# Optimization experiments

Measured on AMD Instinct MI355X. Metric: run time of the kernel, lower is better.

Reference implementation:

```python
import jax, jax.numpy as jnp
import numpy as np
import math

N, LQ, C, HD, L, P = 2, 17821, 256, 8, 4, 4
D = C // HD
SHAPES = [(100, 134), (50, 67), (25, 34), (13, 17)]


def setup_inputs() -> dict:
    key = jax.random.key(0)
    ks = jax.random.split(key, 8)
    shapes = np.array(SHAPES, np.int32)
    areas = shapes[:, 0] * shapes[:, 1]
    starts = np.concatenate([[0], np.cumsum(areas)[:-1]]).astype(np.int32)
    Lin = int(areas.sum())
    sc = 1.0 / math.sqrt(C)
    # sampling_offsets bias: radial grid init as in _reset_parameters
    thetas = np.arange(HD, dtype=np.float32) * (2.0 * math.pi / HD)
    grid = np.stack([np.cos(thetas), np.sin(thetas)], -1)
    grid = grid / np.abs(grid).max(-1, keepdims=True)
    grid = np.tile(grid[:, None, None, :], (1, L, P, 1)) * np.arange(1, P + 1, dtype=np.float32)[None, None, :, None]
    boff = jnp.asarray(grid.reshape(-1), jnp.float32)
    return dict(
        query=jax.random.normal(ks[0], (N, LQ, C), jnp.float32),
        reference_points=jax.random.uniform(ks[1], (N, LQ, L, 2), jnp.float32),
        input_flatten=jax.random.normal(ks[2], (N, Lin, C), jnp.float32),
        input_spatial_shapes=jnp.asarray(shapes),
        input_level_start_index=jnp.asarray(starts),
        Wv=jax.random.normal(ks[3], (C, C), jnp.float32) * sc,
        bv=jnp.zeros((C,), jnp.float32),
        Woff=jax.random.normal(ks[4], (C, HD * L * P * 2), jnp.float32) * 0.01,
        boff=boff,
        Watt=jax.random.normal(ks[5], (C, HD * L * P), jnp.float32) * 0.02,
        batt=jnp.zeros((HD * L * P,), jnp.float32),
        Wout=jax.random.normal(ks[6], (C, C), jnp.float32) * sc,
        bout=jnp.zeros((C,), jnp.float32),
    )


def _ms_deform_attn_core(value, shapes, starts, loc, attw):
    # value: (N, Len_in, HD, D); loc: (N, Lq, HD, L, P, 2) in [0,1]; attw: (N, Lq, HD, L, P)
    n, lq = loc.shape[0], loc.shape[1]
    out = jnp.zeros((n, lq, HD, D), value.dtype)
    for l in range(L):
        H, W = int(shapes[l, 0]), int(shapes[l, 1])
        s = int(starts[l])
        v = value[:, s:s + H * W]                                    # (N, HW, HD, D)
        # (N,Lq,HD,P,2) -> (N,Lq,P,HD,2) -> (N,Lq*P,HD) per coord
        locl = loc[:, :, :, l].transpose(0, 1, 3, 2, 4).reshape(n, lq * P, HD, 2)
        # grid_sample align_corners=False mapping
        x = locl[..., 0] * W - 0.5
        y = locl[..., 1] * H - 0.5
        x0f, y0f = jnp.floor(x), jnp.floor(y)
        fx, fy = x - x0f, y - y0f
        x0, y0 = x0f.astype(jnp.int32), y0f.astype(jnp.int32)

        def corner(xi, yi, w):
            valid = (xi >= 0) & (xi < W) & (yi >= 0) & (yi < H)      # zero padding
            idx = jnp.clip(yi, 0, H - 1) * W + jnp.clip(xi, 0, W - 1)
            g = jnp.take_along_axis(v, idx[..., None], axis=1)        # (N, Lq*P, HD, D)
            return g * (w * valid)[..., None]

        samp = (corner(x0, y0, (1 - fx) * (1 - fy))
                + corner(x0 + 1, y0, fx * (1 - fy))
                + corner(x0, y0 + 1, (1 - fx) * fy)
                + corner(x0 + 1, y0 + 1, fx * fy))                    # (N, Lq*P, HD, D)
        aw = attw[:, :, :, l].transpose(0, 1, 3, 2).reshape(n, lq * P, HD)
        out = out + (samp * aw[..., None]).reshape(n, lq, P, HD, D).sum(axis=2)
    return out.reshape(n, lq, HD * D)


def reference(query, reference_points, input_flatten, input_spatial_shapes,
              input_level_start_index, Wv, bv, Woff, boff, Watt, batt, Wout, bout):
    shapes = np.asarray(input_spatial_shapes)
    starts = np.asarray(input_level_start_index)
    n, lq, _ = query.shape
    value = (input_flatten @ Wv + bv).reshape(n, -1, HD, D)
    offsets = (query @ Woff + boff).reshape(n, lq, HD, L, P, 2)
    # reference_points has last dim 2 -> normalize offsets by (W, H) per level
    norm = jnp.asarray(shapes[:, ::-1], jnp.float32)                  # (L, 2) = (W, H)
    loc = reference_points[:, :, None, :, None, :] + offsets / norm[None, None, None, :, None, :]
    attw = (query @ Watt + batt).reshape(n, lq, HD, L * P)
    attw = jax.nn.softmax(attw, axis=-1).reshape(n, lq, HD, L, P)
    out = _ms_deform_attn_core(value, shapes, starts, loc, attw)
    return out @ Wout + bout
```

## Files before the change

kernel.cpp:

```cpp
#include <hip/hip_runtime.h>
#include <hip/hip_bf16.h>
#include <math.h>

#define NB    2
#define LQ    17821
#define LIN   17821
#define CCH   256
#define HDN   8
#define DCH   32
#define LVL   4
#define NPT   4
#define KDIM  256
#define QCH   16
#define NCHUNK ((LQ + QCH - 1) / QCH)

__constant__ const int   cH[LVL]  = {100, 50, 25, 13};
__constant__ const int   cW[LVL]  = {134, 67, 34, 17};
__constant__ const int   cS[LVL]  = {0, 13400, 16750, 17600};
__constant__ const float cHf[LVL] = {100.f, 50.f, 25.f, 13.f};
__constant__ const float cWf[LVL] = {134.f, 67.f, 34.f, 17.f};
__constant__ const float cRH[LVL] = {1.f/100.f, 1.f/50.f, 1.f/25.f, 1.f/13.f};
__constant__ const float cRW[LVL] = {1.f/134.f, 1.f/67.f, 1.f/34.f, 1.f/17.f};

typedef __attribute__((ext_vector_type(8))) _Float16 f16x8;
typedef __attribute__((ext_vector_type(4))) _Float16 f16x4;
typedef __attribute__((ext_vector_type(2))) _Float16 f16x2;
typedef __attribute__((ext_vector_type(4))) float    f32x4;

__device__ __forceinline__ void glds16(const void* g, void* l) {
    __builtin_amdgcn_global_load_lds(
        (const __attribute__((address_space(1))) void*)g,
        (__attribute__((address_space(3))) void*)l, 16, 0, 0);
}

__device__ __forceinline__ int packw(float w) {
    const unsigned short b = __builtin_bit_cast(unsigned short, (_Float16)w);
    return (int)((unsigned)b * 0x10001u);
}

__global__ void prep_all(const float* __restrict__ Wv,
                         const float* __restrict__ Woff,
                         const float* __restrict__ Watt,
                         const float* __restrict__ Wout,
                         const float* __restrict__ boff,
                         const float* __restrict__ batt,
                         _Float16* __restrict__ wvT,
                         _Float16* __restrict__ wqT,
                         _Float16* __restrict__ wuT,
                         float* __restrict__ b384)
{
    const int i = blockIdx.x * 256 + threadIdx.x;
    if (i < 65536) {
        const int n = i >> 8, k = i & 255;
        wvT[i] = (_Float16)Wv[(size_t)k * 256 + n];
    } else if (i < 131072) {
        const int j = i - 65536, n = j >> 8, k = j & 255;
        wqT[j] = (_Float16)Woff[(size_t)k * 256 + n];
    } else if (i < 163840) {
        const int j = i - 131072, n = j >> 8, k = j & 255;
        wqT[65536 + j] = (_Float16)Watt[(size_t)k * 128 + n];
    } else if (i < 229376) {
        const int j = i - 163840, n = j >> 8, k = j & 255;
        wuT[j] = (_Float16)Wout[(size_t)k * 256 + n];
    } else {
        const int j = i - 229376;
        if (j < 256)      b384[j] = boff[j];
        else if (j < 384) b384[j] = batt[j - 256];
    }
}

template<typename AT, typename OutT, bool PERM>
__device__ __forceinline__ void gemm_body(
    _Float16* AsBase, _Float16* BsBase,
    const AT* __restrict__ A,
    const _Float16* __restrict__ BT,
    const float* __restrict__ bias, OutT* __restrict__ C,
    int M, int Ntot, int bx, int by)
{
    const int t    = threadIdx.x;
    const int wav  = t >> 6;
    const int lane = t & 63;
    const int bm   = by * 128;
    const int bn   = bx * 128;

    const int wr = wav >> 1, wc = wav & 1;
    const int fcol = lane & 15;
    const int fk   = lane >> 4;

    int aoff[4], boff[4];
#pragma unroll
    for (int i = 0; i < 4; ++i) {
        const int ar = wr * 64 + i * 16 + fcol;
        aoff[i] = ar * 64 + ((fk ^ ((ar >> 1) & 3)) << 4);
        const int br = wc * 64 + i * 16 + fcol;
        boff[i] = br * 64 + ((fk ^ ((br >> 1) & 3)) << 4);
    }

    const int srow = lane >> 2;
    const int slot = lane & 3;

    f32x4 acc[4][4];
#pragma unroll
    for (int i = 0; i < 4; ++i)
#pragma unroll
        for (int j = 0; j < 4; ++j) acc[i][j] = (f32x4)(0.f);

    auto stage = [&](int s, int buf) {
        _Float16* As = AsBase + buf * 4096;
        _Float16* Bs = BsBase + buf * 4096;
#pragma unroll
        for (int i = 0; i < 2; ++i) {
            const int j   = wav + i * 4;
            const int row = j * 16 + srow;
            const int swz = ((row >> 1) & 3) << 4;
            const int rga = min(bm + row, M - 1);
            if constexpr (sizeof(AT) == 2) {
                const int kb = (slot << 4) ^ swz;
                glds16((const char*)A + (size_t)rga * 512 + s * 64 + kb,
                       (char*)As + j * 1024);
            } else {
                const char* src = (const char*)A + (size_t)rga * 1024 + s * 128 + slot * 32;
                const float4 u0 = *reinterpret_cast<const float4*>(src);
                const float4 u1 = *reinterpret_cast<const float4*>(src + 16);
                f16x8 hv;
                hv[0] = (_Float16)u0.x; hv[1] = (_Float16)u0.y;
                hv[2] = (_Float16)u0.z; hv[3] = (_Float16)u0.w;
                hv[4] = (_Float16)u1.x; hv[5] = (_Float16)u1.y;
                hv[6] = (_Float16)u1.z; hv[7] = (_Float16)u1.w;
                *reinterpret_cast<f16x8*>((char*)As + j * 1024 + srow * 64
                                          + ((slot << 4) ^ swz)) = hv;
            }
            {
                const int kb = (slot << 4) ^ swz;
                const int rgb = bn + row;
                glds16((const char*)BT + (size_t)rgb * 512 + s * 64 + kb,
                       (char*)Bs + j * 1024);
            }
        }
    };

    stage(0, 0);
    asm volatile("s_waitcnt vmcnt(0) lgkmcnt(0)" ::: "memory");
    __builtin_amdgcn_s_barrier();

    int cur = 0;
#pragma unroll 1
    for (int s = 0; s < 8; ++s) {
        if (s + 1 < 8) {
            stage(s + 1, cur ^ 1);
            if constexpr (sizeof(AT) == 2)
                asm volatile("s_waitcnt vmcnt(4)" ::: "memory");
            else
                asm volatile("s_waitcnt vmcnt(6)" ::: "memory");
            __builtin_amdgcn_sched_barrier(0);
            __builtin_amdgcn_s_barrier();
        }
        const char* As = (const char*)(AsBase + cur * 4096);
        const char* Bs = (const char*)(BsBase + cur * 4096);
        f16x8 af[4], bfr[4];
#pragma unroll
        for (int i = 0; i < 4; ++i) {
            af[i]  = *reinterpret_cast<const f16x8*>(As + aoff[i]);
            bfr[i] = *reinterpret_cast<const f16x8*>(Bs + boff[i]);
        }
        asm volatile("s_waitcnt lgkmcnt(0)" ::: "memory");
        __builtin_amdgcn_sched_barrier(0);
#pragma unroll
        for (int mi = 0; mi < 4; ++mi)
#pragma unroll
            for (int ni = 0; ni < 4; ++ni)
                acc[mi][ni] = __builtin_amdgcn_mfma_f32_16x16x32_f16(
                    af[mi], bfr[ni], acc[mi][ni], 0, 0, 0);
        if (s + 1 < 8)
            __builtin_amdgcn_s_barrier();
        cur ^= 1;
    }

    const int r0 = bm + wr * 64 + (lane >> 4) * 4;
    const int c0 = bn + wc * 64 + fcol;
#pragma unroll
    for (int ni = 0; ni < 4; ++ni) {
        const int col = c0 + ni * 16;
        const float bv = bias[col];
#pragma unroll
        for (int mi = 0; mi < 4; ++mi) {
#pragma unroll
            for (int j = 0; j < 4; ++j) {
                const int r = r0 + mi * 16 + j;
                if (r < M) {
                    const float v = acc[mi][ni][j] + bv;
                    if (PERM) {
                        const int n   = (r >= LIN) ? 1 : 0;
                        const int pos = r - n * LIN;
                        const size_t dst = ((size_t)(n * HDN + (col >> 5)) * LIN + pos) * 32 + (col & 31);
                        C[dst] = (OutT)v;
                    } else {
                        C[(size_t)r * Ntot + col] = (OutT)v;
                    }
                }
            }
        }
    }
}

__global__ __launch_bounds__(256, 3) void gemm_fused2(
    const float* __restrict__ A0, const _Float16* __restrict__ BT0,
    const float* __restrict__ b0, _Float16* __restrict__ C0,
    const float* __restrict__ A1, const _Float16* __restrict__ BT1,
    const float* __restrict__ b1, _Float16* __restrict__ C1, int M)
{
    __shared__ _Float16 As[2][4096];
    __shared__ _Float16 Bs[2][4096];
    if (blockIdx.x < 2)
        gemm_body<float, _Float16, true >(&As[0][0], &Bs[0][0], A0, BT0, b0, C0,
                                          M, 256, blockIdx.x, blockIdx.y);
    else
        gemm_body<float, _Float16, false>(&As[0][0], &Bs[0][0], A1, BT1, b1, C1,
                                          M, 384, blockIdx.x - 2, blockIdx.y);
}

__global__ __launch_bounds__(256, 3) void gemm_out(
    const _Float16* __restrict__ A, const _Float16* __restrict__ BT,
    const float* __restrict__ bias, float* __restrict__ C, int M)
{
    __shared__ _Float16 As[2][4096];
    __shared__ _Float16 Bs[2][4096];
    gemm_body<_Float16, float, false>(&As[0][0], &Bs[0][0], A, BT, bias, C,
                                      M, 256, blockIdx.x, blockIdx.y);
}

__global__ __launch_bounds__(256) void msda_sample(
    const _Float16* __restrict__ value,
    const _Float16* __restrict__ qproj,
    const float* __restrict__ refp,
    _Float16* __restrict__ o16)
{
    __shared__ int2 sIW[QCH * 81 + 4];

    const int t   = threadIdx.x;
    const int bid = blockIdx.x;
    const int chunk = bid % NCHUNK;
    const int nh    = bid / NCHUNK;
    const int h     = nh & 7;
    const int n     = nh >> 3;

    {
        const int q1 = t >> 4;
        const int ip = t & 15;
        const int l  = ip >> 2;

        const int rq  = min(chunk * QCH + q1, LQ - 1);
        const int row = n * LQ + rq;
        const _Float16* qrow = qproj + (size_t)row * 384;

        const float logit = (float)qrow[256 + h * 16 + ip];
        float m = logit;
#pragma unroll
        for (int k = 8; k >= 1; k >>= 1) m = fmaxf(m, __shfl_xor(m, k));
        const float e = __expf(logit - m);
        float s = e;
#pragma unroll
        for (int k = 8; k >= 1; k >>= 1) s += __shfl_xor(s, k);
        const float aw = e / s;

        const float ox = (float)qrow[h * 32 + ip * 2 + 0];
        const float oy = (float)qrow[h * 32 + ip * 2 + 1];
        const float rx = refp[(size_t)row * 8 + l * 2 + 0];
        const float ry = refp[(size_t)row * 8 + l * 2 + 1];

        const int   Ww = cW[l], Hh = cH[l], st = cS[l];
        const float Wf = cWf[l], Hf = cHf[l];
        const float rW = cRW[l], rH = cRH[l];

        const float x = (rx + ox * rW) * Wf - 0.5f;
        const float y = (ry + oy * rH) * Hf - 0.5f;
        const float x0f = floorf(x);
        const float y0f = floorf(y);
        const float fx = x - x0f;
        const float fy = y - y0f;
        const int x0 = (int)x0f, y0 = (int)y0f;
        const int x1 = x0 + 1,   y1 = y0 + 1;

        const bool vx0 = (x0 >= 0) & (x0 < Ww);
        const bool vx1 = (x1 >= 0) & (x1 < Ww);
        const bool vy0 = (y0 >= 0) & (y0 < Hh);
        const bool vy1 = (y1 >= 0) & (y1 < Hh);

        const float gx0 = 1.f - fx, gx1 = fx;
        const float gy0 = 1.f - fy, gy1 = fy;

        const float w00 = (vx0 & vy0) ? gx0 * gy0 * aw : 0.f;
        const float w10 = (vx1 & vy0) ? gx1 * gy0 * aw : 0.f;
        const float w01 = (vx0 & vy1) ? gx0 * gy1 * aw : 0.f;
        const float w11 = (vx1 & vy1) ? gx1 * gy1 * aw : 0.f;

        const int xc0 = min(max(x0, 0), Ww - 1);
        const int xc1 = min(max(x1, 0), Ww - 1);
        const int yc0 = min(max(y0, 0), Hh - 1);
        const int yc1 = min(max(y1, 0), Hh - 1);

        const int base = (nh * LIN + st) * 64;
        const int b0   = q1 * 81 + ip * 5;
        sIW[b0 + 0] = make_int2(base + (yc0 * Ww + xc0) * 64, packw(w00));
        sIW[b0 + 1] = make_int2(base + (yc0 * Ww + xc1) * 64, packw(w10));
        sIW[b0 + 2] = make_int2(base + (yc1 * Ww + xc0) * 64, packw(w01));
        sIW[b0 + 3] = make_int2(base + (yc1 * Ww + xc1) * 64, packw(w11));
    }

    __syncthreads();

    const int q1  = t >> 4;
    const int lv  = (t >> 2) & 3;
    const int sub = t & 3;
    const char* vbase = (const char*)value + sub * 16;

    int2 iw[4][4];
#pragma unroll
    for (int i = 0; i < 4; ++i)
#pragma unroll
        for (int c = 0; c < 4; ++c)
            iw[i][c] = sIW[q1 * 81 + (lv * 4 + i) * 5 + c];

    f16x8 v[4][4];
#pragma unroll
    for (int i = 0; i < 4; ++i)
#pragma unroll
        for (int c = 0; c < 4; ++c)
            v[i][c] = *reinterpret_cast<const f16x8*>(vbase + iw[i][c].x);

    __builtin_amdgcn_sched_barrier(0);

    f16x2 acc2[4] = {};
#pragma unroll
    for (int i = 0; i < 4; ++i) {
#pragma unroll
        for (int c = 0; c < 4; ++c) {
            const f16x2 w2 = __builtin_bit_cast(f16x2, iw[i][c].y);
            const f16x2* v2 = reinterpret_cast<const f16x2*>(&v[i][c]);
#pragma unroll
            for (int j = 0; j < 4; ++j)
                acc2[j] = __builtin_elementwise_fma(v2[j], w2, acc2[j]);
        }
    }

    float acc[8];
#pragma unroll
    for (int j = 0; j < 4; ++j) {
        acc[2 * j]     = (float)acc2[j][0];
        acc[2 * j + 1] = (float)acc2[j][1];
    }

#pragma unroll
    for (int k = 4; k <= 8; k <<= 1)
#pragma unroll
        for (int j = 0; j < 8; ++j)
            acc[j] += __shfl_xor(acc[j], k);

    if ((t & 12) == 0) {
        const int rq  = min(chunk * QCH + q1, LQ - 1);
        const int row = n * LQ + rq;
        const size_t o = (size_t)row * 256 + h * 32 + sub * 8;
        f16x8 hv;
#pragma unroll
        for (int j = 0; j < 8; ++j) hv[j] = (_Float16)acc[j];
        *reinterpret_cast<f16x8*>(&o16[o]) = hv;
    }
}

extern "C" void kernel_launch(void* const* d_in, const int* in_sizes, int n_in,
                              void* d_out, int out_size, void* d_ws, size_t ws_size,
                              hipStream_t stream)
{
    const float* query  = (const float*)d_in[0];
    const float* refp   = (const float*)d_in[1];
    const float* inflat = (const float*)d_in[2];
    const float* Wv     = (const float*)d_in[5];
    const float* bv     = (const float*)d_in[6];
    const float* Woff   = (const float*)d_in[7];
    const float* boff   = (const float*)d_in[8];
    const float* Watt   = (const float*)d_in[9];
    const float* batt   = (const float*)d_in[10];
    const float* Wout   = (const float*)d_in[11];
    const float* bout   = (const float*)d_in[12];
    float* out = (float*)d_out;

    const int M = NB * LQ;
    const size_t MC = (size_t)M * 256;

    float* ws   = (float*)d_ws;
    float* b384 = ws;

    _Float16* fbase = (_Float16*)(b384 + 384);
    _Float16* qp16  = fbase;
    _Float16* v16   = qp16 + (size_t)M * 384;
    _Float16* o16   = v16 + MC;
    _Float16* wvT   = o16 + MC;
    _Float16* wqT   = wvT + 65536;
    _Float16* wuT   = wqT + 98304;

    const dim3 blk(256);
    const int mblk = (M + 127) / 128;

    prep_all<<<dim3(898), blk, 0, stream>>>(Wv, Woff, Watt, Wout, boff, batt,
                                            wvT, wqT, wuT, b384);

    gemm_fused2<<<dim3(5, mblk), blk, 0, stream>>>(
        inflat, wvT, bv, v16,
        query,  wqT, b384, qp16, M);

    msda_sample<<<dim3(NB * HDN * NCHUNK), blk, 0, stream>>>(v16, qp16, refp, o16);

    gemm_out<<<dim3(2, mblk), blk, 0, stream>>>(o16, wuT, bout, out, M);
}
```

Measured before the change: 158.9 us.

## Retile GEMMs to 64-row blocks spanning full output width per block

Replaces the 128x128 GEMM tiles with 64-row tiles covering 256 columns (or 192 for the query projection) per block, with each wavefront owning a column slice. A is then read once per row block instead of once per column tile, which cuts redundant fp32 input reads and the fp16 conversions that go with them. The fp32 A loads are software-pipelined into registers and written to shared memory after the MFMA step, and the barrier and waitcnt placement is reorganised to match. In exchange, each wave does fewer MFMAs per A fragment, blocks use more shared memory for B, and the grid has more, smaller blocks.

After: 149.4 us (median of 2 runs). 1.06x faster.

```diff
diff --git a/kernel.cpp b/kernel.cpp
--- a/kernel.cpp
+++ b/kernel.cpp
@@ -69,9 +69,9 @@
     }
 }
 
-template<typename AT, typename OutT, bool PERM>
-__device__ __forceinline__ void gemm_body(
-    _Float16* AsBase, _Float16* BsBase,
+template<int NWF, typename AT, typename OutT, bool PERM>
+__device__ __forceinline__ void gemm_body64(
+    char* AsB, char* BsB,
     const AT* __restrict__ A,
     const _Float16* __restrict__ BT,
     const float* __restrict__ bias, OutT* __restrict__ C,
@@ -80,106 +80,130 @@
     const int t    = threadIdx.x;
     const int wav  = t >> 6;
     const int lane = t & 63;
-    const int bm   = by * 128;
-    const int bn   = bx * 128;
-
-    const int wr = wav >> 1, wc = wav & 1;
+    const int bm   = by * 64;
+    const int bn   = bx * (NWF * 64);
     const int fcol = lane & 15;
     const int fk   = lane >> 4;
 
-    int aoff[4], boff[4];
+    int aoff[4], boff[NWF];
 #pragma unroll
     for (int i = 0; i < 4; ++i) {
-        const int ar = wr * 64 + i * 16 + fcol;
+        const int ar = i * 16 + fcol;
         aoff[i] = ar * 64 + ((fk ^ ((ar >> 1) & 3)) << 4);
-        const int br = wc * 64 + i * 16 + fcol;
+    }
+#pragma unroll
+    for (int i = 0; i < NWF; ++i) {
+        const int br = wav * (NWF * 16) + i * 16 + fcol;
         boff[i] = br * 64 + ((fk ^ ((br >> 1) & 3)) << 4);
     }
 
     const int srow = lane >> 2;
     const int slot = lane & 3;
 
-    f32x4 acc[4][4];
+    f32x4 acc[4][NWF];
 #pragma unroll
     for (int i = 0; i < 4; ++i)
 #pragma unroll
-        for (int j = 0; j < 4; ++j) acc[i][j] = (f32x4)(0.f);
-
-    auto stage = [&](int s, int buf) {
-        _Float16* As = AsBase + buf * 4096;
-        _Float16* Bs = BsBase + buf * 4096;
-#pragma unroll
-        for (int i = 0; i < 2; ++i) {
+        for (int j = 0; j < NWF; ++j) acc[i][j] = (f32x4)(0.f);
+
+    auto stageB = [&](int s, int buf) {
+#pragma unroll
+        for (int i = 0; i < NWF; ++i) {
             const int j   = wav + i * 4;
             const int row = j * 16 + srow;
-            const int swz = ((row >> 1) & 3) << 4;
-            const int rga = min(bm + row, M - 1);
-            if constexpr (sizeof(AT) == 2) {
-                const int kb = (slot << 4) ^ swz;
-                glds16((const char*)A + (size_t)rga * 512 + s * 64 + kb,
-                       (char*)As + j * 1024);
-            } else {
-                const char* src = (const char*)A + (size_t)rga * 1024 + s * 128 + slot * 32;
-                const float4 u0 = *reinterpret_cast<const float4*>(src);
-                const float4 u1 = *reinterpret_cast<const float4*>(src + 16);
-                f16x8 hv;
-                hv[0] = (_Float16)u0.x; hv[1] = (_Float16)u0.y;
-                hv[2] = (_Float16)u0.z; hv[3] = (_Float16)u0.w;
-                hv[4] = (_Float16)u1.x; hv[5] = (_Float16)u1.y;
-                hv[6] = (_Float16)u1.z; hv[7] = (_Float16)u1.w;
-                *reinterpret_cast<f16x8*>((char*)As + j * 1024 + srow * 64
-                                          + ((slot << 4) ^ swz)) = hv;
-            }
-            {
-                const int kb = (slot << 4) ^ swz;
-                const int rgb = bn + row;
-                glds16((const char*)BT + (size_t)rgb * 512 + s * 64 + kb,
-                       (char*)Bs + j * 1024);
-            }
+            const int kb  = (slot << 4) ^ (((row >> 1) & 3) << 4);
+            glds16((const char*)BT + (size_t)(bn + row) * 512 + s * 64 + kb,
+                   BsB + buf * (NWF * 4096) + j * 1024);
         }
     };
-
-    stage(0, 0);
-    asm volatile("s_waitcnt vmcnt(0) lgkmcnt(0)" ::: "memory");
-    __builtin_amdgcn_s_barrier();
+    auto stageA16 = [&](int s, int buf) {
+        const int row = wav * 16 + srow;
+        const int kb  = (slot << 4) ^ (((row >> 1) & 3) << 4);
+        const int rga = min(bm + row, M - 1);
+        glds16((const char*)A + (size_t)rga * 512 + s * 64 + kb,
+               AsB + buf * 4096 + wav * 1024);
+    };
+
+    const int arow = t >> 2;
+    const int rga32 = min(bm + arow, M - 1);
+    const char* aSrc = (const char*)A + (size_t)rga32 * 1024 + slot * 32;
+    const int aDst = arow * 64 + ((slot << 4) ^ (((arow >> 1) & 3) << 4));
+
+    float4 a0, a1;
+    auto loadA32 = [&](int s) {
+        a0 = *reinterpret_cast<const float4*>(aSrc + s * 128);
+        a1 = *reinterpret_cast<const float4*>(aSrc + s * 128 + 16);
+    };
+    auto writeA32 = [&](int buf) {
+        f16x8 hv;
+        hv[0] = (_Float16)a0.x; hv[1] = (_Float16)a0.y;
+        hv[2] = (_Float16)a0.z; hv[3] = (_Float16)a0.w;
+        hv[4] = (_Float16)a1.x; hv[5] = (_Float16)a1.y;
+        hv[6] = (_Float16)a1.z; hv[7] = (_Float16)a1.w;
+        *reinterpret_cast<f16x8*>(AsB + buf * 4096 + aDst) = hv;
+    };
+
+    if constexpr (sizeof(AT) == 2) {
+        stageA16(0, 0);
+        stageB(0, 0);
+    } else {
+        loadA32(0);
+        stageB(0, 0);
+        writeA32(0);
+    }
 
     int cur = 0;
 #pragma unroll 1
     for (int s = 0; s < 8; ++s) {
-        if (s + 1 < 8) {
-            stage(s + 1, cur ^ 1);
-            if constexpr (sizeof(AT) == 2)
-                asm volatile("s_waitcnt vmcnt(4)" ::: "memory");
-            else
-                asm volatile("s_waitcnt vmcnt(6)" ::: "memory");
-            __builtin_amdgcn_sched_barrier(0);
-            __builtin_amdgcn_s_barrier();
+        if (s < 7) {
+            if constexpr (sizeof(AT) == 2) {
+                stageA16(s + 1, cur ^ 1);
+                stageB(s + 1, cur ^ 1);
+            } else {
+                loadA32(s + 1);
+                stageB(s + 1, cur ^ 1);
+            }
+            if constexpr (sizeof(AT) == 2) {
+                if constexpr (NWF == 4) asm volatile("s_waitcnt vmcnt(5) lgkmcnt(0)" ::: "memory");
+                else                    asm volatile("s_waitcnt vmcnt(4) lgkmcnt(0)" ::: "memory");
+            } else {
+                if constexpr (NWF == 4) asm volatile("s_waitcnt vmcnt(6) lgkmcnt(0)" ::: "memory");
+                else                    asm volatile("s_waitcnt vmcnt(5) lgkmcnt(0)" ::: "memory");
+            }
+        } else {
+            asm volatile("s_waitcnt vmcnt(0) lgkmcnt(0)" ::: "memory");
         }
-        const char* As = (const char*)(AsBase + cur * 4096);
-        const char* Bs = (const char*)(BsBase + cur * 4096);
-        f16x8 af[4], bfr[4];
-#pragma unroll
-        for (int i = 0; i < 4; ++i) {
-            af[i]  = *reinterpret_cast<const f16x8*>(As + aoff[i]);
+        __builtin_amdgcn_sched_barrier(0);
+        __builtin_amdgcn_s_barrier();
+
+        const char* As = AsB + cur * 4096;
+        const char* Bs = BsB + cur * (NWF * 4096);
+        f16x8 af[4], bfr[NWF];
+#pragma unroll
+        for (int i = 0; i < 4; ++i)
+            af[i] = *reinterpret_cast<const f16x8*>(As + aoff[i]);
+#pragma unroll
+        for (int i = 0; i < NWF; ++i)
             bfr[i] = *reinterpret_cast<const f16x8*>(Bs + boff[i]);
-        }
         asm volatile("s_waitcnt lgkmcnt(0)" ::: "memory");
         __builtin_amdgcn_sched_barrier(0);
 #pragma unroll
         for (int mi = 0; mi < 4; ++mi)
 #pragma unroll
-            for (int ni = 0; ni < 4; ++ni)
+            for (int ni = 0; ni < NWF; ++ni)
                 acc[mi][ni] = __builtin_amdgcn_mfma_f32_16x16x32_f16(
                     af[mi], bfr[ni], acc[mi][ni], 0, 0, 0);
-        if (s + 1 < 8)
-            __builtin_amdgcn_s_barrier();
+        __builtin_amdgcn_s_barrier();
+        if (s < 7) {
+            if constexpr (sizeof(AT) != 2) writeA32(cur ^ 1);
+        }
         cur ^= 1;
     }
 
-    const int r0 = bm + wr * 64 + (lane >> 4) * 4;
-    const int c0 = bn + wc * 64 + fcol;
-#pragma unroll
-    for (int ni = 0; ni < 4; ++ni) {
+    const int r0 = bm + (lane >> 4) * 4;
+    const int c0 = bn + wav * (NWF * 16) + fcol;
+#pragma unroll
+    for (int ni = 0; ni < NWF; ++ni) {
         const int col = c0 + ni * 16;
         const float bv = bias[col];
 #pragma unroll
@@ -209,24 +233,24 @@
     const float* __restrict__ A1, const _Float16* __restrict__ BT1,
     const float* __restrict__ b1, _Float16* __restrict__ C1, int M)
 {
-    __shared__ _Float16 As[2][4096];
-    __shared__ _Float16 Bs[2][4096];
-    if (blockIdx.x < 2)
-        gemm_body<float, _Float16, true >(&As[0][0], &Bs[0][0], A0, BT0, b0, C0,
-                                          M, 256, blockIdx.x, blockIdx.y);
+    __shared__ _Float16 As[2 * 2048];
+    __shared__ _Float16 Bs[2 * 8192];
+    if (blockIdx.x == 0)
+        gemm_body64<4, float, _Float16, true >((char*)As, (char*)Bs, A0, BT0, b0, C0,
+                                               M, 256, 0, blockIdx.y);
     else
-        gemm_body<float, _Float16, false>(&As[0][0], &Bs[0][0], A1, BT1, b1, C1,
-                                          M, 384, blockIdx.x - 2, blockIdx.y);
+        gemm_body64<3, float, _Float16, false>((char*)As, (char*)Bs, A1, BT1, b1, C1,
+                                               M, 384, blockIdx.x - 1, blockIdx.y);
 }
 
 __global__ __launch_bounds__(256, 3) void gemm_out(
     const _Float16* __restrict__ A, const _Float16* __restrict__ BT,
     const float* __restrict__ bias, float* __restrict__ C, int M)
 {
-    __shared__ _Float16 As[2][4096];
-    __shared__ _Float16 Bs[2][4096];
-    gemm_body<_Float16, float, false>(&As[0][0], &Bs[0][0], A, BT, bias, C,
-                                      M, 256, blockIdx.x, blockIdx.y);
+    __shared__ _Float16 As[2 * 2048];
+    __shared__ _Float16 Bs[2 * 8192];
+    gemm_body64<4, _Float16, float, false>((char*)As, (char*)Bs, A, BT, bias, C,
+                                           M, 256, 0, blockIdx.y);
 }
 
 __global__ __launch_bounds__(256) void msda_sample(
@@ -399,16 +423,16 @@
     _Float16* wuT   = wqT + 98304;
 
     const dim3 blk(256);
-    const int mblk = (M + 127) / 128;
+    const int mblk64 = (M + 63) / 64;
 
     prep_all<<<dim3(898), blk, 0, stream>>>(Wv, Woff, Watt, Wout, boff, batt,
                                             wvT, wqT, wuT, b384);
 
-    gemm_fused2<<<dim3(5, mblk), blk, 0, stream>>>(
+    gemm_fused2<<<dim3(3, mblk64), blk, 0, stream>>>(
         inflat, wvT, bv, v16,
         query,  wqT, b384, qp16, M);
 
     msda_sample<<<dim3(NB * HDN * NCHUNK), blk, 0, stream>>>(v16, qp16, refp, o16);
 
-    gemm_out<<<dim3(2, mblk), blk, 0, stream>>>(o16, wuT, bout, out, M);
-}
+    gemm_out<<<dim3(1, mblk64), blk, 0, stream>>>(o16, wuT, bout, out, M);
+}
```
